# Kernel optimization log

Measured on AMD Instinct MI355X. Metric: run time of the kernel, lower is better.

## Reference

```python
import jax, jax.numpy as jnp
import numpy as np

N_DOC, N_WORD, N_ENT, N_POS = 10000, 20000, 10000, 60
D, D_POS_IN, D_WEMB = 128, 60, 300
E11, E22, E33, E01, E02, E03 = 320000, 160000, 3600, 300000, 100000, 150000
EPS = 1e-9


def spmm(rows, cols, vals, x, n_out):
    """Sparse (n_out x n_in) adjacency @ x via gather + weighted segment-sum."""
    return jax.ops.segment_sum(vals[:, None] * x[cols], rows, num_segments=n_out)


def gcn(rows, cols, vals, x, n_out, W=None, b=None):
    """GCN layer: adj @ (x W + b) with ReLU; identity=True in torch == W is None."""
    h = x if W is None else x @ W + b
    return jax.nn.relu(spmm(rows, cols, vals, h, n_out))


def setup_inputs():
    key = jax.random.key(0)
    ks = iter(jax.random.split(key, 64))
    randn = lambda s: jax.random.normal(next(ks), s, jnp.float32)
    rand = lambda s: jax.random.uniform(next(ks), s, dtype=jnp.float32)
    ridx = lambda s, hi: jax.random.randint(next(ks), s, 0, hi, jnp.int32)
    return {
        "f1": randn((N_WORD, D)),
        "f2": randn((N_ENT, D)),
        "f3": randn((N_POS, D_POS_IN)),
        "word_emb": randn((N_ENT, D_WEMB)),
        "a11_rows": ridx((E11,), N_WORD), "a11_cols": ridx((E11,), N_WORD), "a11_vals": rand((E11,)),
        "a22_rows": ridx((E22,), N_ENT), "a22_cols": ridx((E22,), N_ENT), "a22_vals": rand((E22,)),
        "a33_rows": ridx((E33,), N_POS), "a33_cols": ridx((E33,), N_POS), "a33_vals": rand((E33,)),
        "a01_rows": ridx((E01,), N_DOC), "a01_cols": ridx((E01,), N_WORD), "a01_vals": rand((E01,)),
        "a02_rows": ridx((E02,), N_DOC), "a02_cols": ridx((E02,), N_ENT), "a02_vals": rand((E02,)),
        "a03_rows": ridx((E03,), N_DOC), "a03_cols": ridx((E03,), N_POS), "a03_vals": rand((E03,)),
        "W3": randn((D_POS_IN, D)) * 0.1, "b3": jnp.zeros((D,), jnp.float32),
        "W1_2": randn((D, D)) * 0.1, "b1_2": jnp.zeros((D,), jnp.float32),
        "W2_2": randn((D, D)) * 0.1, "b2_2": jnp.zeros((D,), jnp.float32),
        "W3_2": randn((D, D)) * 0.1, "b3_2": jnp.zeros((D,), jnp.float32),
    }


def reference(f1, f2, f3, word_emb,
              a11_rows, a11_cols, a11_vals, a22_rows, a22_cols, a22_vals,
              a33_rows, a33_cols, a33_vals, a01_rows, a01_cols, a01_vals,
              a02_rows, a02_cols, a02_vals, a03_rows, a03_cols, a03_vals,
              W3, b3, W1_2, b1_2, W2_2, b2_2, W3_2, b3_2):
    # eval mode: F.dropout(training=False) is a no-op
    # type 1 (words): GCN(identity=True) -> GCN_2
    h1 = gcn(a11_rows, a11_cols, a11_vals, f1, N_WORD)
    h1 = gcn(a11_rows, a11_cols, a11_vals, h1, N_WORD, W1_2, b1_2)
    # type 2 (entities, concat_word_emb=True): GCN(identity=True) -> GCN_2 -> concat word_emb
    h2 = gcn(a22_rows, a22_cols, a22_vals, f2, N_ENT)
    h2 = gcn(a22_rows, a22_cols, a22_vals, h2, N_ENT, W2_2, b2_2)
    h2 = jnp.concatenate([h2, word_emb], axis=-1)  # [N_ENT, D + D_WEMB]
    # type 3 (POS): full GCN -> GCN_2
    h3 = gcn(a33_rows, a33_cols, a33_vals, f3, N_POS, W3, b3)
    h3 = gcn(a33_rows, a33_cols, a33_vals, h3, N_POS, W3_2, b3_2)
    # cross-type aggregation onto documents + L2 normalization
    outs = []
    for rows, cols, vals, h in ((a01_rows, a01_cols, a01_vals, h1),
                                (a02_rows, a02_cols, a02_vals, h2),
                                (a03_rows, a03_cols, a03_vals, h3)):
        agg = spmm(rows, cols, vals, h, N_DOC)  # [N_DOC, d]
        outs.append(agg / (jnp.linalg.norm(agg, axis=-1, keepdims=True) + EPS))
    return tuple(outs)
```

## Files before the change

### kernel.cpp

```cpp
#include <hip/hip_runtime.h>
#include <hip/hip_bf16.h>

typedef __hip_bfloat16 bf16;

#define N_DOC   10000
#define N_WORD  20000
#define N_ENT   10000
#define N_POS   60
#define DD      128
#define D_WEMB  300
#define E11     320000
#define E22     160000
#define E33     3600
#define E01     300000
#define E02     100000
#define E03     150000

#define ROFF11  0
#define ROFF22  20000
#define ROFF33  30000
#define ROFF01  30060
#define ROFF02  40060
#define ROFF03  50060
#define NROWS   60060
// ... 129 lines not shown
    int j = tid & 127;
    int row = row0 + q;
    float* xrh = xr + q * K;
    if (row < N_POS && j < K) {
        float x = loadf(X, (size_t)row * K + j, xisb);
        if (RELU) x = fmaxf(x, 0.f);
        xrh[j] = x;
    }
    __syncthreads();
    if (row >= N_POS) return;
    float acc = loadf(b, j, isb);
    #pragma unroll 8
    for (int k = 0; k < K; ++k)
        acc = fmaf(xrh[k], loadf(W, (size_t)k * 128 + j, isb), acc);
    storef(out, (size_t)row * 128 + j, oisb, acc);
}

__global__ __launch_bounds__(512) void bin_edges_fused(
        const int* __restrict__ r11, const int* __restrict__ c11, const void* __restrict__ v11,
        const int* __restrict__ r22, const int* __restrict__ c22, const void* __restrict__ v22,
        const int* __restrict__ r33, const int* __restrict__ c33, const void* __restrict__ v33,
        const int* __restrict__ r01, const int* __restrict__ c01, const void* __restrict__ v01,
        const int* __restrict__ r02, const int* __restrict__ c02, const void* __restrict__ v02,
        const int* __restrict__ r03, const int* __restrict__ c03, const void* __restrict__ v03,
        int* __restrict__ bcur, uint2* __restrict__ staging,
        const void* __restrict__ f1, const void* __restrict__ f2, const void* __restrict__ wemb,
        unsigned* __restrict__ f1q, unsigned* __restrict__ f2q, unsigned* __restrict__ wq,
        const void* __restrict__ f3, const void* __restrict__ W3, const void* __restrict__ b3,
        void* __restrict__ P3a,
        const int* __restrict__ dflag) {
    __shared__ int smem_i[3 * NBUCK];
    int* hist   = smem_i;
    int* gbase  = smem_i + NBUCK;
    int* cursor = smem_i + 2 * NBUCK;
    int blk = blockIdx.x;
    int t = threadIdx.x;
    if (blk < NB1K) {
        if (t < NBUCK) { hist[t] = 0; cursor[t] = 0; }
        __syncthreads();
        int isb = *dflag;
        int base0 = blk * P1_TILE;
        unsigned rx[P1_EPT], ry[P1_EPT];
        int bk[P1_EPT];
        #pragma unroll
        for (int k = 0; k < P1_EPT; ++k) {
            int i = base0 + t + k * 512;
            bk[k] = -1;
            if (i < NEDGES) {
                int slot, col; float val;
                edge_decode(i, r11, c11, v11, r22, c22, v22, r33, c33, v33,
                            r01, c01, v01, r02, c02, v02, r03, c03, v03,
                            isb, slot, col, val);
                rx[k] = ((unsigned)slot << 16) | (unsigned)col;
                ry[k] = f2b(val);
                bk[k] = slot >> BSHIFT;
                atomicAdd(&hist[bk[k]], 1);
            }
        }
        __syncthreads();
        if (t < NBUCK) {
            int c = hist[t];
            gbase[t] = c ? atomicAdd(bcur + t, c) : 0;
        }
        __syncthreads();
        #pragma unroll
        for (int k = 0; k < P1_EPT; ++k) {
            if (bk[k] >= 0) {
                int p = atomicAdd(&cursor[bk[k]], 1);
                int dst = gbase[bk[k]] + p;
                if (dst < (bk[k] + 1) * BCAP)
                    staging[dst] = make_uint2(rx[k], ry[k]);
            }
        }
    } else if (blk < NB1K + NCONV) {
        int isb = *dflag;
        int tid = (blk - NB1K) * 512 + t;
        int stride = NCONV * 512;
        conv_seg(f1,   f1q, N_WORD * (DD / 2),     isb, tid, stride);
        conv_seg(f2,   f2q, N_ENT  * (DD / 2),     isb, tid, stride);
        conv_seg(wemb, wq,  N_ENT  * (D_WEMB / 2), isb, tid, stride);
    } else {
        int isb = *dflag;
        int row0 = (blk - NB1K - NCONV) * 4;
        rowpar_body512<false, 60>(f3, isb, W3, b3, P3a, isb, isb, row0, t, (float*)smem_i);
    }
}

__global__ __launch_bounds__(512) void finalize_csr(
        const int* __restrict__ bcur, const uint2* __restrict__ staging,
        int* __restrict__ G, unsigned* __restrict__ pairs) {
    __shared__ int h[512], rp[512], cu[512];
    __shared__ int wsum2[8], wtop[2], bbs[2];
    int b = blockIdx.x, t = threadIdx.x;
    int lane = t & 63, w = t >> 6;
    h[t] = 0;
    int cnt_t = 0, s = 0;
    if (t < NBUCK) {
        int c = bcur[t] - t * BCAP;
        cnt_t = (c < BCAP) ? c : BCAP;
    }
    if (t < 128) {
        s = cnt_t;
        #pragma unroll
        for (int off = 1; off < 64; off <<= 1) {
            int y = __shfl_up(s, off);
            if (lane >= off) s += y;
        }
        if (lane == 63) wtop[w] = s;
    }
    __syncthreads();
    if (t == b) {
        bbs[0] = ((w > 0) ? wtop[0] : 0) + s - cnt_t;
        bbs[1] = cnt_t;
    }
    if (b == NBUCK - 1 && t == NBUCK - 1)
        G[NROWS] = ((w > 0) ? wtop[0] : 0) + s;
    __syncthreads();
    int bb = bbs[0];
    int cnt = bbs[1];
    const uint2* st = staging + (size_t)b * BCAP;
    for (int i = t; i < cnt; i += 512)
        atomicAdd(&h[(st[i].x >> 16) & 511], 1);
    __syncthreads();
    int x = h[t];
    s = x;
    #pragma unroll
    for (int off = 1; off < 64; off <<= 1) {
        int y = __shfl_up(s, off);
        if (lane >= off) s += y;
    }
    if (lane == 63) wsum2[w] = s;
    __syncthreads();
    if (t < 8) {
        int v = wsum2[t];
        #pragma unroll
        for (int off = 1; off < 8; off <<= 1) {
            int y = __shfl_up(v, off);
            if (lane >= off) v += y;
        }
        wsum2[t] = v;
    }
    __syncthreads();
    int myrp = ((w > 0) ? wsum2[w - 1] : 0) + s - x;
    rp[t] = myrp;
    cu[t] = 0;
    int slot = (b << BSHIFT) + t;
    if (slot < NROWS) G[slot] = bb + myrp;
    __syncthreads();
    for (int i = t; i < cnt; i += 512) {
        uint2 r = st[i];
        int sl = (r.x >> 16) & 511;
        int p = atomicAdd(&cu[sl], 1);
        pairs[bb + rp[sl] + p] = (r.y << 16) | (r.x & 0xffffu);
    }
}

__global__ void hist2_kernel(const int* __restrict__ rowsA, int nEA,
                             const int* __restrict__ rowsB, int nEB,
                             int nA, int* __restrict__ cnt) {
    int i = blockIdx.x * blockDim.x + threadIdx.x;
    if (i < nEA) atomicAdd(cnt + rowsA[i], 1);
    else if (i < nEA + nEB) atomicAdd(cnt + nA + rowsB[i - nEA], 1);
}

__device__ void scan_ex(const int* __restrict__ cnt, int* __restrict__ rp, int n) {
    __shared__ int wsum[16];
    __shared__ int carry;
    int t = threadIdx.x, lane = t & 63, w = t >> 6;
    if (t == 0) carry = 0;
    __syncthreads();
    for (int base = 0; base < n; base += 1024) {
        int i = base + t;
        int x = (i < n) ? cnt[i] : 0;
        int s = x;
        #pragma unroll
        for (int off = 1; off < 64; off <<= 1) {
            int y = __shfl_up(s, off);
            if (lane >= off) s += y;
        }
        if (lane == 63) wsum[w] = s;
        __syncthreads();
        if (w == 0) {
            int v = (lane < 16) ? wsum[lane] : 0;
            #pragma unroll
            for (int off = 1; off < 16; off <<= 1) {
                int y = __shfl_up(v, off);
                if (lane >= off) v += y;
            }
            if (lane < 16) wsum[lane] = v;
        }
        __syncthreads();
        int woff = (w > 0) ? wsum[w - 1] : 0;
        if (i < n) rp[i] = carry + woff + s - x;
        __syncthreads();
        if (t == 0) carry += wsum[15];
        __syncthreads();
    }
    if (t == 0) rp[n] = carry;
}

__global__ __launch_bounds__(1024) void scan2_kernel(
        const int* __restrict__ cntA, int* __restrict__ rpA, int nA,
        const int* __restrict__ cntB, int* __restrict__ rpB, int nB) {
    scan_ex(cntA, rpA, nA);
    __syncthreads();
    scan_ex(cntB, rpB, nB);
}

__global__ void copy2_kernel(const int* __restrict__ rpA, const int* __restrict__ rpB,
                             int nA, int nB, int* __restrict__ cur) {
    int i = blockIdx.x * blockDim.x + threadIdx.x;
    if (i < nA) cur[i] = rpA[i];
    else if (i < nA + nB) cur[i] = rpB[i - nA];
}

__global__ void scatter2_kernel(const int* __restrict__ rowsA, const int* __restrict__ colsA,
                                const void* __restrict__ valsA, int nEA,
                                const int* __restrict__ rowsB, const int* __restrict__ colsB,
                                const void* __restrict__ valsB, int nEB,
                                int nA, int* __restrict__ cur,
                                unsigned* __restrict__ pairsA, unsigned* __restrict__ pairsB,
                                const int* __restrict__ dflag) {
    int i = blockIdx.x * blockDim.x + threadIdx.x;
    int isb = *dflag;
    if (i < nEA) {
        int p = atomicAdd(cur + rowsA[i], 1);
        pairsA[p] = pack_pair(colsA[i], loadf(valsA, i, isb));
    } else if (i < nEA + nEB) {
        int k = i - nEA;
        int p = atomicAdd(cur + nA + rowsB[k], 1);
        pairsB[p] = pack_pair(colsB[k], loadf(valsB, k, isb));
    }
}

template<bool RELU>
__device__ __forceinline__ void gather_accum16(
        const int* __restrict__ rp, const unsigned* __restrict__ pairs,
        const void* __restrict__ src, int sisb, int row, int lane,
        float& tx, float& ty) {
    int e0 = rp[row], e1 = rp[row + 1];
    float accx[8], accy[8];
    #pragma unroll
    for (int k = 0; k < 8; ++k) { accx[k] = 0.f; accy[k] = 0.f; }
    int e = e0;
    if (sisb) {
        const bf16* sb = (const bf16*)src;
        for (; e + 16 <= e1; e += 16) {
            unsigned p[16], u[16];
            #pragma unroll
            for (int k = 0; k < 16; ++k) p[k] = pairs[e + k];
            #pragma unroll
            for (int k = 0; k < 16; ++k)
                u[k] = ((const unsigned*)(sb + (size_t)(p[k] & 0xffffu) * 128))[lane];
            #pragma unroll
            for (int k = 0; k < 16; ++k) {
                float v = b2f(p[k] >> 16);
                float x0 = b2f(u[k] & 0xffffu), x1 = b2f(u[k] >> 16);
                if (RELU) { x0 = fmaxf(x0, 0.f); x1 = fmaxf(x1, 0.f); }
                accx[k & 7] = fmaf(v, x0, accx[k & 7]);
                accy[k & 7] = fmaf(v, x1, accy[k & 7]);
            }
        }
        for (; e + 8 <= e1; e += 8) {
            unsigned p[8], u[8];
            #pragma unroll
            for (int k = 0; k < 8; ++k) p[k] = pairs[e + k];
            #pragma unroll
            for (int k = 0; k < 8; ++k)
                u[k] = ((const unsigned*)(sb + (size_t)(p[k] & 0xffffu) * 128))[lane];
            #pragma unroll
            for (int k = 0; k < 8; ++k) {
                float v = b2f(p[k] >> 16);
                float x0 = b2f(u[k] & 0xffffu), x1 = b2f(u[k] >> 16);
                if (RELU) { x0 = fmaxf(x0, 0.f); x1 = fmaxf(x1, 0.f); }
                accx[k] = fmaf(v, x0, accx[k]);
                accy[k] = fmaf(v, x1, accy[k]);
            }
        }
        for (; e + 2 <= e1; e += 2) {
            unsigned p0 = pairs[e], p1 = pairs[e + 1];
            unsigned u0 = ((const unsigned*)(sb + (size_t)(p0 & 0xffffu) * 128))[lane];
            unsigned u1 = ((const unsigned*)(sb + (size_t)(p1 & 0xffffu) * 128))[lane];
            float v0 = b2f(p0 >> 16), v1 = b2f(p1 >> 16);
            float x0 = b2f(u0 & 0xffffu), x1 = b2f(u0 >> 16);
            float y0 = b2f(u1 & 0xffffu), y1 = b2f(u1 >> 16);
            if (RELU) {
                x0 = fmaxf(x0, 0.f); x1 = fmaxf(x1, 0.f);
                y0 = fmaxf(y0, 0.f); y1 = fmaxf(y1, 0.f);
            }
            accx[0] = fmaf(v0, x0, accx[0]); accy[0] = fmaf(v0, x1, accy[0]);
            accx[1] = fmaf(v1, y0, accx[1]); accy[1] = fmaf(v1, y1, accy[1]);
        }
        if (e < e1) {
            unsigned p = pairs[e];
            float v = b2f(p >> 16);
            unsigned u = ((const unsigned*)(sb + (size_t)(p & 0xffffu) * 128))[lane];
            float x0 = b2f(u & 0xffffu), x1 = b2f(u >> 16);
            if (RELU) { x0 = fmaxf(x0, 0.f); x1 = fmaxf(x1, 0.f); }
            accx[0] = fmaf(v, x0, accx[0]); accy[0] = fmaf(v, x1, accy[0]);
        }
    } else {
        const float* sf = (const float*)src;
        for (; e + 16 <= e1; e += 16) {
            unsigned p[16]; float2 u[16];
            #pragma unroll
            for (int k = 0; k < 16; ++k) p[k] = pairs[e + k];
            #pragma unroll
            for (int k = 0; k < 16; ++k)
                u[k] = ((const float2*)(sf + (size_t)(p[k] & 0xffffu) * 128))[lane];
            #pragma unroll
            for (int k = 0; k < 16; ++k) {
                float v = b2f(p[k] >> 16);
                float x0 = u[k].x, x1 = u[k].y;
                if (RELU) { x0 = fmaxf(x0, 0.f); x1 = fmaxf(x1, 0.f); }
                accx[k & 7] = fmaf(v, x0, accx[k & 7]);
                accy[k & 7] = fmaf(v, x1, accy[k & 7]);
            }
        }
        for (; e + 8 <= e1; e += 8) {
            unsigned p[8]; float2 u[8];
            #pragma unroll
            for (int k = 0; k < 8; ++k) p[k] = pairs[e + k];
            #pragma unroll
            for (int k = 0; k < 8; ++k)
                u[k] = ((const float2*)(sf + (size_t)(p[k] & 0xffffu) * 128))[lane];
            #pragma unroll
            for (int k = 0; k < 8; ++k) {
                float v = b2f(p[k] >> 16);
                float x0 = u[k].x, x1 = u[k].y;
                if (RELU) { x0 = fmaxf(x0, 0.f); x1 = fmaxf(x1, 0.f); }
                accx[k] = fmaf(v, x0, accx[k]);
                accy[k] = fmaf(v, x1, accy[k]);
            }
        }
        for (; e + 2 <= e1; e += 2) {
            unsigned p0 = pairs[e], p1 = pairs[e + 1];
            float2 x = ((const float2*)(sf + (size_t)(p0 & 0xffffu) * 128))[lane];
            float2 y = ((const float2*)(sf + (size_t)(p1 & 0xffffu) * 128))[lane];
            float v0 = b2f(p0 >> 16), v1 = b2f(p1 >> 16);
            if (RELU) {
                x.x = fmaxf(x.x, 0.f); x.y = fmaxf(x.y, 0.f);
                y.x = fmaxf(y.x, 0.f); y.y = fmaxf(y.y, 0.f);
            }
            accx[0] = fmaf(v0, x.x, accx[0]); accy[0] = fmaf(v0, x.y, accy[0]);
            accx[1] = fmaf(v1, y.x, accx[1]); accy[1] = fmaf(v1, y.y, accy[1]);
        }
        if (e < e1) {
            unsigned p = pairs[e];
            float v = b2f(p >> 16);
            float2 x = ((const float2*)(sf + (size_t)(p & 0xffffu) * 128))[lane];
            if (RELU) { x.x = fmaxf(x.x, 0.f); x.y = fmaxf(x.y, 0.f); }
            accx[0] = fmaf(v, x.x, accx[0]); accy[0] = fmaf(v, x.y, accy[0]);
        }
    }
    tx = ((accx[0] + accx[1]) + (accx[2] + accx[3])) + ((accx[4] + accx[5]) + (accx[6] + accx[7]));
    ty = ((accy[0] + accy[1]) + (accy[2] + accy[3])) + ((accy[4] + accy[5]) + (accy[6] + accy[7]));
}

template<bool RELU>
__device__ __forceinline__ void gather128_body(
        const int* __restrict__ rp, const unsigned* __restrict__ pairs,
        const void* __restrict__ src, int sisb,
        void* __restrict__ dst, int disb, int row, int lane) {
    float tx, ty;
    gather_accum16<RELU>(rp, pairs, src, sisb, row, lane, tx, ty);
    if (disb) {
        ((unsigned*)((bf16*)dst + (size_t)row * 128))[lane] = f2b(tx) | (f2b(ty) << 16);
    } else {
        ((float2*)((float*)dst + (size_t)row * 128))[lane] = make_float2(tx, ty);
    }
}

template<bool RELU>
__device__ __forceinline__ void norm128_body(
        const int* __restrict__ rp, const unsigned* __restrict__ pairs,
        const void* __restrict__ src, int sisb,
        void* __restrict__ out, size_t elem_off, int row, int lane, int isb) {
    float tx, ty;
    gather_accum16<RELU>(rp, pairs, src, sisb, row, lane, tx, ty);
    float ss = tx * tx + ty * ty;
    #pragma unroll
    for (int off = 32; off > 0; off >>= 1) ss += __shfl_down(ss, off);
    ss = __shfl(ss, 0);
    float inv = 1.0f / (sqrtf(ss) + 1e-9f);
    size_t base = elem_off + (size_t)row * 128;
    if (isb) {
        ((unsigned*)((bf16*)out + base))[lane] = f2b(tx * inv) | (f2b(ty * inv) << 16);
    } else {
        ((float2*)((float*)out + base))[lane] = make_float2(tx * inv, ty * inv);
    }
}

__device__ __forceinline__ void norm428_body(
        const int* __restrict__ rp, const unsigned* __restrict__ pairs,
        const void* __restrict__ src1, int s1b,
        const void* __restrict__ src2, int s2b,
        void* __restrict__ out, size_t elem_off, int row, int lane, int isb) {
    constexpr int P2 = D_WEMB / 2;
    int e0 = rp[row], e1 = rp[row + 1];
    float2 a1 = make_float2(0.f, 0.f), b1 = make_float2(0.f, 0.f);
    float2 a2[3], b2v[3];
// ... 63 lines not shown
        }
        x0 = fmaxf(x0, 0.f); x1 = fmaxf(x1, 0.f);
        a1.x = fmaf(v, x0, a1.x); a1.y = fmaf(v, x1, a1.y);
        if (s2b) {
            const unsigned* sp = (const unsigned*)((const bf16*)src2 + (size_t)c * D_WEMB);
            #pragma unroll
            for (int s = 0; s < 3; ++s) {
                int pi = lane + 64 * s;
                if (pi < P2) {
                    unsigned u = sp[pi];
                    a2[s].x = fmaf(v, b2f(u & 0xffffu), a2[s].x);
                    a2[s].y = fmaf(v, b2f(u >> 16),     a2[s].y);
                }
            }
        } else {
            const float2* sp = (const float2*)((const float*)src2 + (size_t)c * D_WEMB);
            #pragma unroll
            for (int s = 0; s < 3; ++s) {
                int pi = lane + 64 * s;
                if (pi < P2) {
                    float2 x = sp[pi];
                    a2[s].x = fmaf(v, x.x, a2[s].x);
                    a2[s].y = fmaf(v, x.y, a2[s].y);
                }
            }
        }
    }
    float t1x = a1.x + b1.x, t1y = a1.y + b1.y;
    float t2x[3], t2y[3];
    #pragma unroll
    for (int s = 0; s < 3; ++s) { t2x[s] = a2[s].x + b2v[s].x; t2y[s] = a2[s].y + b2v[s].y; }
    float ss = t1x * t1x + t1y * t1y;
    #pragma unroll
    for (int s = 0; s < 3; ++s) {
        int pi = lane + 64 * s;
        if (pi < P2) ss += t2x[s] * t2x[s] + t2y[s] * t2y[s];
    }
    #pragma unroll
    for (int off = 32; off > 0; off >>= 1) ss += __shfl_down(ss, off);
    ss = __shfl(ss, 0);
    float inv = 1.0f / (sqrtf(ss) + 1e-9f);
    size_t base = elem_off + (size_t)row * (DD + D_WEMB);
    if (isb) {
        ((unsigned*)((bf16*)out + base))[lane] = f2b(t1x * inv) | (f2b(t1y * inv) << 16);
        unsigned* o2 = (unsigned*)((bf16*)out + base + DD);
        #pragma unroll
        for (int s = 0; s < 3; ++s) {
            int pi = lane + 64 * s;
            if (pi < P2) o2[pi] = f2b(t2x[s] * inv) | (f2b(t2y[s] * inv) << 16);
        }
    } else {
        ((float2*)((float*)out + base))[lane] = make_float2(t1x * inv, t1y * inv);
        float2* o2 = (float2*)((float*)out + base + DD);
        #pragma unroll
        for (int s = 0; s < 3; ++s) {
            int pi = lane + 64 * s;
            if (pi < P2) o2[pi] = make_float2(t2x[s] * inv, t2y[s] * inv);
        }
    }
}

template<bool RELU>
__global__ void spmm_gather128(const int* __restrict__ rowptr, const unsigned* __restrict__ pairs,
                               const void* __restrict__ src, int src_flagged,
                               void* __restrict__ dst, int dst_flagged,
                               int n, const int* __restrict__ dflag) {
    int row = blockIdx.x * 4 + (threadIdx.x >> 6);
    if (row >= n) return;
    int isb = *dflag;
    gather128_body<RELU>(rowptr, pairs, src, src_flagged ? isb : 0,
                         dst, dst_flagged ? isb : 0, row, threadIdx.x & 63);
}

__global__ void hop_posg(const int* __restrict__ G, const unsigned* __restrict__ pairs,
                         int roff1, const void* __restrict__ src1, void* __restrict__ dst1, int n1, int B1,
                         int roff2, const void* __restrict__ src2, void* __restrict__ dst2, int n2, int B2,
                         const void* __restrict__ Psrc, void* __restrict__ Pdst,
                         const int* __restrict__ dflag) {
    int b = blockIdx.x;
    int lane = threadIdx.x & 63;
    if (b < B1) {
        int row = b * 4 + (threadIdx.x >> 6);
        if (row >= n1) return;
        gather128_body<false>(G + roff1, pairs, src1, 1, dst1, 1, row, lane);
    } else if (b < B1 + B2) {
        int row = (b - B1) * 4 + (threadIdx.x >> 6);
        if (row >= n2) return;
        gather128_body<false>(G + roff2, pairs, src2, 1, dst2, 1, row, lane);
    } else {
        int isb = *dflag;
        int row = (b - B1 - B2) * 4 + (threadIdx.x >> 6);
        if (row >= N_POS) return;
        gather128_body<false>(G + ROFF33, pairs, Psrc, isb, Pdst, isb, row, lane);
    }
}

template<bool RELU>
__global__ void spmm_norm128(const int* __restrict__ rowptr, const unsigned* __restrict__ pairs,
                             const void* __restrict__ src, int src_flagged,
                             void* __restrict__ out, size_t elem_off,
                             int n, const int* __restrict__ dflag) {
    int row = blockIdx.x * 4 + (threadIdx.x >> 6);
    if (row >= n) return;
    int isb = *dflag;
    norm128_body<RELU>(rowptr, pairs, src, src_flagged ? isb : 0, out, elem_off,
                       row, threadIdx.x & 63, isb);
}

__global__ void spmm2_norm(const int* __restrict__ rowptr, const unsigned* __restrict__ pairs,
                           const void* __restrict__ src1, int s1_flagged,
                           const void* __restrict__ src2, int s2_flagged,
                           void* __restrict__ out, size_t elem_off,
                           int n, const int* __restrict__ dflag) {
    int row = blockIdx.x * 4 + (threadIdx.x >> 6);
    if (row >= n) return;
    int isb = *dflag;
    norm428_body(rowptr, pairs, src1, s1_flagged ? isb : 0, src2, s2_flagged ? isb : 0,
                 out, elem_off, row, threadIdx.x & 63, isb);
}

__global__ void final_norm_all(const int* __restrict__ G, const unsigned* __restrict__ pairs,
                               const void* __restrict__ s1, const void* __restrict__ e0b,
                               const void* __restrict__ wemb, const void* __restrict__ p3b,
                               void* __restrict__ out,
                               size_t off1, size_t off2, size_t off3,
                               const int* __restrict__ dflag) {
    int isb = *dflag;
    int lane = threadIdx.x & 63;
    int b = blockIdx.x;
    if (b < 2500) {
        int row = b * 4 + (threadIdx.x >> 6);
        if (row >= N_DOC) return;
        norm128_body<true>(G + ROFF01, pairs, s1, 1, out, off1, row, lane, isb);
    } else if (b < 5000) {
        int row = (b - 2500) * 4 + (threadIdx.x >> 6);
        if (row >= N_DOC) return;
        norm428_body(G + ROFF02, pairs, e0b, 1, wemb, 1, out, off2, row, lane, isb);
    } else {
        int row = (b - 5000) * 4 + (threadIdx.x >> 6);
        if (row >= N_DOC) return;
        norm128_body<true>(G + ROFF03, pairs, p3b, isb, out, off3, row, lane, isb);
    }
}

template<bool RELU>
__global__ void spmm_kernel(const int* __restrict__ rows, const int* __restrict__ cols,
                            const void* __restrict__ vals,
                            const void* __restrict__ src, int sstride, int src_flagged,
                            float* __restrict__ dst, int dstride, int doff,
                            int d, int nE, const int* __restrict__ dflag) {
    int e = blockIdx.x * (blockDim.x >> 6) + (threadIdx.x >> 6);
    if (e >= nE) return;
    int isb  = *dflag;
    int sisb = src_flagged ? isb : 0;
    int lane = threadIdx.x & 63;
    int r = rows[e];
    int c = cols[e];
    float v = loadf(vals, e, isb);
    size_t sbase = (size_t)c * sstride;
    float* dp = dst + (size_t)r * dstride + doff;
    if (sisb) {
        const unsigned* sp = (const unsigned*)((const bf16*)src + sbase);
        for (int j = 2 * lane; j < d; j += 128) {
            unsigned u = sp[j >> 1];
            float x0 = b2f(u & 0xffffu);
            float x1 = b2f(u >> 16);
            if (RELU) { x0 = fmaxf(x0, 0.f); x1 = fmaxf(x1, 0.f); }
            atomicAdd(dp + j,     v * x0);
            atomicAdd(dp + j + 1, v * x1);
        }
    } else {
        const float2* sp = (const float2*)((const float*)src + sbase);
        for (int j = 2 * lane; j < d; j += 128) {
            float2 x = sp[j >> 1];
            if (RELU) { x.x = fmaxf(x.x, 0.f); x.y = fmaxf(x.y, 0.f); }
            atomicAdd(dp + j,     v * x.x);
            atomicAdd(dp + j + 1, v * x.y);
        }
    }
}

template<bool RELU, bool XB>
__device__ __forceinline__ void gemm_tile_body(
        const void* __restrict__ X, const void* __restrict__ W,
        const void* __restrict__ b, void* __restrict__ out, int n,
        int bx, int by, int isb, int oisb, float* Wl ) {
    if (bx * 64 >= n) return;
    int tid = threadIdx.x;
    int jc = by * 64;
    if (isb) {
        const uint2* Wg = (const uint2*)W;
        float4* Wl4 = (float4*)Wl;
        for (int vidx = tid; vidx < 2048; vidx += 256) {
            int k = vidx >> 4, jl4 = vidx & 15;
            uint2 u = Wg[k * 32 + (jc >> 2) + jl4];
            float4 vv;
            vv.x = b2f(u.x & 0xffffu);
            vv.y = b2f(u.x >> 16);
            vv.z = b2f(u.y & 0xffffu);
            vv.w = b2f(u.y >> 16);
            Wl4[vidx] = vv;
        }
    } else {
        const float4* Wg = (const float4*)W;
        float4* Wl4 = (float4*)Wl;
        for (int vidx = tid; vidx < 2048; vidx += 256) {
            int k = vidx >> 4, jl4 = vidx & 15;
            Wl4[vidx] = Wg[k * 32 + (jc >> 2) + jl4];
        }
    }
    __syncthreads();
    int j2 = tid & 31;
    int g  = tid >> 5;
    float bc0 = loadf(b, jc + 2 * j2, isb);
    float bc1 = loadf(b, jc + 2 * j2 + 1, isb);
    int i0 = bx * 64 + g * 8;
    float a0[8], a1[8];
    #pragma unroll
    for (int r = 0; r < 8; ++r) { a0[r] = bc0; a1[r] = bc1; }
    const char* xbase = (const char*)X + (size_t)i0 * 128 * (XB ? 2 : 4);
    const float2* Wl2 = (const float2*)Wl;
    #pragma unroll 2
    for (int k4 = 0; k4 < 32; ++k4) {
        float2 w0 = Wl2[(4 * k4 + 0) * 32 + j2];
        float2 w1 = Wl2[(4 * k4 + 1) * 32 + j2];
        float2 w2 = Wl2[(4 * k4 + 2) * 32 + j2];
        float2 w3 = Wl2[(4 * k4 + 3) * 32 + j2];
        #pragma unroll
        for (int r = 0; r < 8; ++r) {
            float4 v;
            if (XB) {
                uint2 u = ((const uint2*)xbase)[r * 32 + k4];
                v.x = b2f(u.x & 0xffffu); v.y = b2f(u.x >> 16);
                v.z = b2f(u.y & 0xffffu); v.w = b2f(u.y >> 16);
            } else {
                v = ((const float4*)xbase)[r * 32 + k4];
            }
            if (RELU) {
                v.x = fmaxf(v.x, 0.f); v.y = fmaxf(v.y, 0.f);
                v.z = fmaxf(v.z, 0.f); v.w = fmaxf(v.w, 0.f);
            }
            a0[r] = fmaf(v.w, w3.x, fmaf(v.z, w2.x, fmaf(v.y, w1.x, fmaf(v.x, w0.x, a0[r]))));
            a1[r] = fmaf(v.w, w3.y, fmaf(v.z, w2.y, fmaf(v.y, w1.y, fmaf(v.x, w0.y, a1[r]))));
        }
    }
    #pragma unroll
    for (int r = 0; r < 8; ++r) {
        int i = i0 + r;
        if (i < n) {
            if (oisb) {
                ((unsigned*)((bf16*)out + (size_t)i * 128 + jc))[j2] =
                    f2b(a0[r]) | (f2b(a1[r]) << 16);
            } else {
                ((float2*)((float*)out + (size_t)i * 128 + jc))[j2] =
                    make_float2(a0[r], a1[r]);
            }
        }
    }
}

template<bool RELU>
__global__ __launch_bounds__(256) void gemm_tile(
        const float* __restrict__ X, const void* __restrict__ W,
        const void* __restrict__ b, void* __restrict__ out, int n,
        const int* __restrict__ dflag) {
    __shared__ float Wl[128 * 64];
    int isb = *dflag;
    gemm_tile_body<RELU, false>(X, W, b, out, n, blockIdx.x, blockIdx.y, isb, isb, Wl);
}

template<bool RELU>
__global__ __launch_bounds__(256) void gemm_tile_b2g(
        const void* __restrict__ X1, const void* __restrict__ W1, const void* __restrict__ b1,
        void* __restrict__ out1, int n1, int G1,
        const void* __restrict__ X2, const void* __restrict__ W2, const void* __restrict__ b2,
        void* __restrict__ out2, int n2, int GT,
        const void* __restrict__ PX, const void* __restrict__ PW,
        const void* __restrict__ Pb, void* __restrict__ PO,
        const int* __restrict__ dflag) {
    __shared__ float Wl[128 * 64];
    int isb = *dflag;
    int x = blockIdx.x;
    if (x < G1) {
        gemm_tile_body<RELU, true>(X1, W1, b1, out1, n1, x, blockIdx.y, isb, 1, Wl);
    } else if (x < GT) {
        gemm_tile_body<RELU, true>(X2, W2, b2, out2, n2, x - G1, blockIdx.y, isb, 1, Wl);
    } else {
        if (blockIdx.y != 0) return;
        int row = (x - GT) * 2 + (threadIdx.x >> 7);
        rowpar_body256<true, 128>(PX, isb, PW, Pb, PO, isb, isb, row, threadIdx.x, Wl);
    }
}

template<bool RELU>
__global__ __launch_bounds__(256) void gemm128_kernel(
        const float* __restrict__ X, const void* __restrict__ W,
        const void* __restrict__ b, float* __restrict__ out, int n,
        const int* __restrict__ dflag) {
    __shared__ float Wl[128 * 128];
    int isb = *dflag;
    int tid = threadIdx.x;
    if (isb) {
        const uint2* Wg = (const uint2*)W;
        float4* Wl4 = (float4*)Wl;
        for (int idx = tid; idx < 4096; idx += 256) {
            uint2 u = Wg[idx];
            float4 vv;
            vv.x = b2f(u.x & 0xffffu);
            vv.y = b2f(u.x >> 16);
            vv.z = b2f(u.y & 0xffffu);
            vv.w = b2f(u.y >> 16);
            Wl4[idx] = vv;
        }
    } else {
        const float4* Wg = (const float4*)W;
        float4* Wl4 = (float4*)Wl;
        for (int idx = tid; idx < 4096; idx += 256) Wl4[idx] = Wg[idx];
    }
    __syncthreads();
    int j = tid & 127;
    int h = tid >> 7;
    float bj = loadf(b, j, isb);
    int row0 = blockIdx.x * 64 + h * 32;
    for (int q = 0; q < 8; ++q) {
        int gi = row0 + q * 4;
        if (gi >= n) break;
        const float4* x0 = (const float4*)(X + (size_t)gi * 128);
        const float4* x1 = x0 + 32;
        const float4* x2 = x1 + 32;
        const float4* x3 = x2 + 32;
        float a0 = bj, a1 = bj, a2 = bj, a3 = bj;
        #pragma unroll 4
        for (int k4 = 0; k4 < 32; ++k4) {
            float4 v0 = x0[k4], v1 = x1[k4], v2 = x2[k4], v3 = x3[k4];
            if (RELU) {
                v0.x = fmaxf(v0.x, 0.f); v0.y = fmaxf(v0.y, 0.f); v0.z = fmaxf(v0.z, 0.f); v0.w = fmaxf(v0.w, 0.f);
                v1.x = fmaxf(v1.x, 0.f); v1.y = fmaxf(v1.y, 0.f); v1.z = fmaxf(v1.z, 0.f); v1.w = fmaxf(v1.w, 0.f);
                v2.x = fmaxf(v2.x, 0.f); v2.y = fmaxf(v2.y, 0.f); v2.z = fmaxf(v2.z, 0.f); v2.w = fmaxf(v2.w, 0.f);
                v3.x = fmaxf(v3.x, 0.f); v3.y = fmaxf(v3.y, 0.f); v3.z = fmaxf(v3.z, 0.f); v3.w = fmaxf(v3.w, 0.f);
            }
            float w0 = Wl[(4 * k4 + 0) * 128 + j];
            float w1 = Wl[(4 * k4 + 1) * 128 + j];
            float w2 = Wl[(4 * k4 + 2) * 128 + j];
            float w3 = Wl[(4 * k4 + 3) * 128 + j];
            a0 = fmaf(v0.w, w3, fmaf(v0.z, w2, fmaf(v0.y, w1, fmaf(v0.x, w0, a0))));
            a1 = fmaf(v1.w, w3, fmaf(v1.z, w2, fmaf(v1.y, w1, fmaf(v1.x, w0, a1))));
            a2 = fmaf(v2.w, w3, fmaf(v2.z, w2, fmaf(v2.y, w1, fmaf(v2.x, w0, a2))));
            a3 = fmaf(v3.w, w3, fmaf(v3.z, w2, fmaf(v3.y, w1, fmaf(v3.x, w0, a3))));
        }
        float* o = out + (size_t)gi * 128 + j;
        o[0] = a0; o[128] = a1; o[256] = a2; o[384] = a3;
    }
}

template<bool RELU, int K>
__global__ void rowpar_gemm(const void* __restrict__ X, int x_flagged,
                            const void* __restrict__ W, const void* __restrict__ b,
                            void* __restrict__ out, int out_flagged,
                            const int* __restrict__ dflag) {
    __shared__ float xr[K];
    int isb  = *dflag;
    int xisb = x_flagged ? isb : 0;
    int oisb = out_flagged ? isb : 0;
    int row = blockIdx.x;
    int j = threadIdx.x;
    if (j < K) {
        float x = loadf(X, (size_t)row * K + j, xisb);
        if (RELU) x = fmaxf(x, 0.f);
        xr[j] = x;
    }
    __syncthreads();
    float acc = loadf(b, j, isb);
    #pragma unroll 8
// ... 71 lines not shown
        for (int j = 2 * lane; j < d; j += 128) {
            float2 x = a2[j >> 1];
            o[j >> 1] = make_float2(x.x * inv, x.y * inv);
        }
    }
}

static inline int spmm_grid(int nE) { return (nE + 3) / 4; }
static inline int row_grid(int n)   { return (n + 3) / 4; }
static inline int pad8(int x)       { return (x + 7) & ~7; }

static void build2(hipStream_t stream,
                   const int* rowsA, const int* colsA, const void* valsA, int nA, int nEA,
                   const int* rowsB, const int* colsB, const void* valsB, int nB, int nEB,
                   int* rpA, int* rpB, int* curAB, unsigned* pairsA, unsigned* pairsB,
                   const int* dflag) {
    int nE = nEA + nEB;
    hipMemsetAsync(curAB, 0, (size_t)(nA + nB) * 4, stream);
    hist2_kernel<<<(nE + 255) / 256, 256, 0, stream>>>(rowsA, nEA, rowsB, nEB, nA, curAB);
    scan2_kernel<<<1, 1024, 0, stream>>>(curAB, rpA, nA, curAB + nA, rpB, nB);
    copy2_kernel<<<(nA + nB + 255) / 256, 256, 0, stream>>>(rpA, rpB, nA, nB, curAB);
    scatter2_kernel<<<(nE + 255) / 256, 256, 0, stream>>>(
        rowsA, colsA, valsA, nEA, rowsB, colsB, valsB, nEB, nA, curAB, pairsA, pairsB, dflag);
}

extern "C" void kernel_launch(void* const* d_in, const int* in_sizes, int n_in,
                              void* d_out, int out_size, void* d_ws, size_t ws_size,
                              hipStream_t stream) {
    const void* f1   = d_in[0];
    const void* f2   = d_in[1];
    const void* f3   = d_in[2];
    const void* wemb = d_in[3];
    const int*  a11r = (const int*)d_in[4];
    const int*  a11c = (const int*)d_in[5];
    const void* a11v = d_in[6];
    const int*  a22r = (const int*)d_in[7];
    const int*  a22c = (const int*)d_in[8];
    const void* a22v = d_in[9];
    const int*  a33r = (const int*)d_in[10];
    const int*  a33c = (const int*)d_in[11];
    const void* a33v = d_in[12];
    const int*  a01r = (const int*)d_in[13];
    const int*  a01c = (const int*)d_in[14];
    const void* a01v = d_in[15];
    const int*  a02r = (const int*)d_in[16];
    const int*  a02c = (const int*)d_in[17];
    const void* a02v = d_in[18];
    const int*  a03r = (const int*)d_in[19];
    const int*  a03c = (const int*)d_in[20];
    const void* a03v = d_in[21];
    const void* W3   = d_in[22];
    const void* b3   = d_in[23];
    const void* W1_2 = d_in[24];
    const void* b1_2 = d_in[25];
    const void* W2_2 = d_in[26];
    const void* b2_2 = d_in[27];
    const void* W3_2 = d_in[28];
    const void* b3_2 = d_in[29];

    int*   dflag = (int*)d_ws;
    float* base  = (float*)d_ws + 16;

    const size_t OUT1_OFF = 0;
    const size_t OUT2_OFF = (size_t)N_DOC * DD;
    const size_t OUT3_OFF = OUT2_OFF + (size_t)N_DOC * (DD + D_WEMB);

    dim3 blk(256);

    const size_t WS_BIG = 64 + (size_t)HFO_END * 4;
    const size_t WS_MID = 64 + 22240000ull + (60008ull + 620000ull) * 4;

    if (ws_size >= WS_BIG) {
        uint2*    staging = (uint2*)(base + HFO_STAGE);
        unsigned* pairs   = (unsigned*)(base + HFO_PAIRS);
        int*      G       = (int*)(base + HFO_G);
        int*      bcur    = (int*)(base + HFO_BCUR);
        void*     f1q     = (void*)(base + HFO_F1B);
        void*     f2q     = (void*)(base + HFO_F2B);
        void*     wq      = (void*)(base + HFO_WEMBB);
        void*     S0b     = (void*)(base + HFO_S0B);
        void*     S1b     = (void*)(base + HFO_S1B);
        void*     E0b     = (void*)(base + HFO_E0B);
        void*     E1b     = (void*)(base + HFO_E1B);
        float*    P3a     = base + HFO_P3A;
        float*    P3b     = base + HFO_P3B;

        detect_kernel<<<1, 256, 0, stream>>>((const unsigned*)f1, dflag, bcur);

        bin_edges_fused<<<NB1K + NCONV + NPOSB1, 512, 0, stream>>>(
            a11r, a11c, a11v, a22r, a22c, a22v, a33r, a33c, a33v,
            a01r, a01c, a01v, a02r, a02c, a02v, a03r, a03c, a03v,
            bcur, staging,
            f1, f2, wemb, (unsigned*)f1q, (unsigned*)f2q, (unsigned*)wq,
            f3, W3, b3, P3a, dflag);

        finalize_csr<<<NBUCK, 512, 0, stream>>>(bcur, staging, G, pairs);

        int B1 = row_grid(N_WORD), B2 = row_grid(N_ENT);
        hop_posg<<<B1 + B2 + row_grid(N_POS), blk, 0, stream>>>(
            G, pairs, ROFF11, f1q, S0b, N_WORD, B1,
            ROFF22, f2q, E0b, N_ENT, B2, P3a, P3b, dflag);
        {
            int G1 = pad8((N_WORD + 63) / 64), G2 = pad8((N_ENT + 63) / 64);
            int GT = G1 + G2;
            gemm_tile_b2g<true><<<dim3(GT + 30, 2), 256, 0, stream>>>(
                S0b, W1_2, b1_2, S1b, N_WORD, G1,
                E0b, W2_2, b2_2, E1b, N_ENT, GT,
                P3b, W3_2, b3_2, P3a, dflag);
        }
        hop_posg<<<B1 + B2 + row_grid(N_POS), blk, 0, stream>>>(
            G, pairs, ROFF11, S1b, S0b, N_WORD, B1,
            ROFF22, E1b, E0b, N_ENT, B2, P3a, P3b, dflag);

        final_norm_all<<<7500, blk, 0, stream>>>(
            G, pairs, S0b, E0b, wq, P3b, d_out, OUT1_OFF, OUT2_OFF, OUT3_OFF, dflag);
    } else if (ws_size >= WS_MID) {
        detect_kernel<<<1, 256, 0, stream>>>((const unsigned*)f1, dflag, (int*)nullptr);
        float* S0   = base;
        float* S1   = base + 2560000;
        float* E0   = base;
        float* E1   = base + 1280000;
        float* P3a  = base;
        float* P3b  = base + 7680;
        int* I = (int*)(base + 5560000);
        {
            int* rpA = I; int* rpB = rpA + (N_WORD + 1); int* cur = rpB + (N_DOC + 1);
            unsigned* pA = (unsigned*)(cur + N_WORD + N_DOC); unsigned* pB = pA + E11;
            build2(stream, a11r, a11c, a11v, N_WORD, E11,
                   a01r, a01c, a01v, N_DOC, E01, rpA, rpB, cur, pA, pB, dflag);
            spmm_gather128<false><<<row_grid(N_WORD), blk, 0, stream>>>(
                rpA, pA, f1, 1, S0, 0, N_WORD, dflag);
            gemm_tile<true><<<dim3(pad8((N_WORD + 63) / 64), 2), 256, 0, stream>>>(
                S0, W1_2, b1_2, S1, N_WORD, dflag);
            spmm_gather128<false><<<row_grid(N_WORD), blk, 0, stream>>>(
                rpA, pA, S1, 1, S0, 1, N_WORD, dflag);
            spmm_norm128<true><<<row_grid(N_DOC), blk, 0, stream>>>(
                rpB, pB, S0, 1, d_out, OUT1_OFF, N_DOC, dflag);
        }
        {
            int* rpA = I; int* rpB = rpA + (N_ENT + 1); int* cur = rpB + (N_DOC + 1);
            unsigned* pA = (unsigned*)(cur + N_ENT + N_DOC); unsigned* pB = pA + E22;
            build2(stream, a22r, a22c, a22v, N_ENT, E22,
                   a02r, a02c, a02v, N_DOC, E02, rpA, rpB, cur, pA, pB, dflag);
            spmm_gather128<false><<<row_grid(N_ENT), blk, 0, stream>>>(
                rpA, pA, f2, 1, E0, 0, N_ENT, dflag);
            gemm_tile<true><<<dim3(pad8((N_ENT + 63) / 64), 2), 256, 0, stream>>>(
                E0, W2_2, b2_2, E1, N_ENT, dflag);
            spmm_gather128<false><<<row_grid(N_ENT), blk, 0, stream>>>(
                rpA, pA, E1, 1, E0, 1, N_ENT, dflag);
            spmm2_norm<<<row_grid(N_DOC), blk, 0, stream>>>(
                rpB, pB, E0, 1, wemb, 1, d_out, OUT2_OFF, N_DOC, dflag);
        }
        {
            int* rpA = I; int* rpB = rpA + (N_POS + 1); int* cur = rpB + (N_DOC + 1);
            unsigned* pA = (unsigned*)(cur + N_POS + N_DOC); unsigned* pB = pA + E33;
            build2(stream, a33r, a33c, a33v, N_POS, E33,
                   a03r, a03c, a03v, N_DOC, E03, rpA, rpB, cur, pA, pB, dflag);
            rowpar_gemm<false, 60><<<N_POS, 128, 0, stream>>>(
                f3, 1, W3, b3, P3a, 1, dflag);
            spmm_gather128<false><<<row_grid(N_POS), blk, 0, stream>>>(
                rpA, pA, P3a, 1, P3b, 1, N_POS, dflag);
            rowpar_gemm<true, 128><<<N_POS, 128, 0, stream>>>(
                P3b, 1, W3_2, b3_2, P3a, 1, dflag);
            spmm_gather128<false><<<row_grid(N_POS), blk, 0, stream>>>(
                rpA, pA, P3a, 1, P3b, 1, N_POS, dflag);
            spmm_norm128<true><<<row_grid(N_DOC), blk, 0, stream>>>(
                rpB, pB, P3b, 1, d_out, OUT3_OFF, N_DOC, dflag);
        }
// ... 58 lines not shown
```

Measured before the change: 286.8 us.

## Use 16-byte quarter-wave gathers for bf16 SpMM rows and store POS features as bf16

Adds gather4 helpers in which each wavefront splits into four 16-lane groups. Each group loads a whole 256-byte bf16 row with uint4 loads, and the partial sums are combined with cross-lane shuffles. This replaces the old scheme where each lane loaded 4 bytes per edge, and it is used for the hop gathers and two of the normalization paths. The POS intermediates are now always written and read as bf16, whatever the input dtype, so the new path applies to them too. The 16-edge unrolled loops in the old gather are dropped. Wider loads mean fewer memory transactions, at the cost of shuffle reductions, tail masking and extra bf16 rounding on the POS path.

```diff
diff --git a/kernel.cpp b/kernel.cpp
--- a/kernel.cpp
+++ b/kernel.cpp
@@ -235,7 +235,7 @@
     } else {
         int isb = *dflag;
         int row0 = (blk - NB1K - NCONV) * 4;
-        rowpar_body512<false, 60>(f3, isb, W3, b3, P3a, isb, isb, row0, t, (float*)smem_i);
+        rowpar_body512<false, 60>(f3, isb, W3, b3, P3a, 1, isb, row0, t, (float*)smem_i);
     }
 }
 
@@ -386,6 +386,112 @@
     }
 }
 
+__device__ __forceinline__ void accum8_bf16(uint4 u, float v, bool relu, float* acc) {
+    float x0 = b2f(u.x & 0xffffu), x1 = b2f(u.x >> 16);
+    float x2 = b2f(u.y & 0xffffu), x3 = b2f(u.y >> 16);
+    float x4 = b2f(u.z & 0xffffu), x5 = b2f(u.z >> 16);
+    float x6 = b2f(u.w & 0xffffu), x7 = b2f(u.w >> 16);
+    if (relu) {
+        x0 = fmaxf(x0, 0.f); x1 = fmaxf(x1, 0.f); x2 = fmaxf(x2, 0.f); x3 = fmaxf(x3, 0.f);
+        x4 = fmaxf(x4, 0.f); x5 = fmaxf(x5, 0.f); x6 = fmaxf(x6, 0.f); x7 = fmaxf(x7, 0.f);
+    }
+    acc[0] = fmaf(v, x0, acc[0]); acc[1] = fmaf(v, x1, acc[1]);
+    acc[2] = fmaf(v, x2, acc[2]); acc[3] = fmaf(v, x3, acc[3]);
+    acc[4] = fmaf(v, x4, acc[4]); acc[5] = fmaf(v, x5, acc[5]);
+    acc[6] = fmaf(v, x6, acc[6]); acc[7] = fmaf(v, x7, acc[7]);
+}
+
+template<bool RELU>
+__device__ __forceinline__ void gather4_accum(
+        const int* __restrict__ rp, const unsigned* __restrict__ pairs,
+        const bf16* __restrict__ src, int row, int lane, float* acc) {
+    #pragma unroll
+    for (int j = 0; j < 8; ++j) acc[j] = 0.f;
+    int e0 = rp[row], e1 = rp[row + 1];
+    if (e0 >= e1) return;
+    int q = lane >> 4, sub = lane & 15;
+    int e = e0;
+    for (; e + 16 <= e1; e += 16) {
+        unsigned p0 = pairs[e + q];
+        unsigned p1 = pairs[e + 4 + q];
+        unsigned p2 = pairs[e + 8 + q];
+        unsigned p3 = pairs[e + 12 + q];
+        uint4 u0 = *(const uint4*)((const unsigned short*)src + (size_t)(p0 & 0xffffu) * 128 + sub * 8);
+        uint4 u1 = *(const uint4*)((const unsigned short*)src + (size_t)(p1 & 0xffffu) * 128 + sub * 8);
+        uint4 u2 = *(const uint4*)((const unsigned short*)src + (size_t)(p2 & 0xffffu) * 128 + sub * 8);
+        uint4 u3 = *(const uint4*)((const unsigned short*)src + (size_t)(p3 & 0xffffu) * 128 + sub * 8);
+        accum8_bf16(u0, b2f(p0 >> 16), RELU, acc);
+        accum8_bf16(u1, b2f(p1 >> 16), RELU, acc);
+        accum8_bf16(u2, b2f(p2 >> 16), RELU, acc);
+        accum8_bf16(u3, b2f(p3 >> 16), RELU, acc);
+    }
+    for (; e < e1; e += 4) {
+        int idx = e + q;
+        unsigned p = pairs[(idx < e1) ? idx : (e1 - 1)];
+        float v = (idx < e1) ? b2f(p >> 16) : 0.f;
+        uint4 u = *(const uint4*)((const unsigned short*)src + (size_t)(p & 0xffffu) * 128 + sub * 8);
+        accum8_bf16(u, v, RELU, acc);
+    }
+}
+
+template<bool RELU>
+__device__ __forceinline__ void gather4_body(
+        const int* __restrict__ rp, const unsigned* __restrict__ pairs,
+        const bf16* __restrict__ src, bf16* __restrict__ dst, int row, int lane) {
+    float acc[8];
+    gather4_accum<RELU>(rp, pairs, src, row, lane, acc);
+    #pragma unroll
+    for (int j = 0; j < 8; ++j) {
+        acc[j] += __shfl_xor(acc[j], 16);
+        acc[j] += __shfl_xor(acc[j], 32);
+    }
+    if ((lane >> 4) == 0) {
+        int sub = lane & 15;
+        uint4 o;
+        o.x = f2b(acc[0]) | (f2b(acc[1]) << 16);
+        o.y = f2b(acc[2]) | (f2b(acc[3]) << 16);
+        o.z = f2b(acc[4]) | (f2b(acc[5]) << 16);
+        o.w = f2b(acc[6]) | (f2b(acc[7]) << 16);
+        *(uint4*)((unsigned short*)dst + (size_t)row * 128 + sub * 8) = o;
+    }
+}
+
+template<bool RELU>
+__device__ __forceinline__ void norm4_body(
+        const int* __restrict__ rp, const unsigned* __restrict__ pairs,
+        const bf16* __restrict__ src, void* __restrict__ out, size_t elem_off,
+        int row, int lane, int oisb) {
+    float acc[8];
+    gather4_accum<RELU>(rp, pairs, src, row, lane, acc);
+    #pragma unroll
+    for (int j = 0; j < 8; ++j) {
+        acc[j] += __shfl_xor(acc[j], 16);
+        acc[j] += __shfl_xor(acc[j], 32);
+    }
+    float ss = 0.f;
+    #pragma unroll
+    for (int j = 0; j < 8; ++j) ss = fmaf(acc[j], acc[j], ss);
+    #pragma unroll
+    for (int off = 1; off < 16; off <<= 1) ss += __shfl_xor(ss, off);
+    float inv = 1.0f / (sqrtf(ss) + 1e-9f);
+    if ((lane >> 4) == 0) {
+        int sub = lane & 15;
+        size_t base = elem_off + (size_t)row * 128;
+        if (oisb) {
+            uint4 o;
+            o.x = f2b(acc[0] * inv) | (f2b(acc[1] * inv) << 16);
+            o.y = f2b(acc[2] * inv) | (f2b(acc[3] * inv) << 16);
+            o.z = f2b(acc[4] * inv) | (f2b(acc[5] * inv) << 16);
+            o.w = f2b(acc[6] * inv) | (f2b(acc[7] * inv) << 16);
+            *(uint4*)((unsigned short*)out + base + sub * 8) = o;
+        } else {
+            float4* op = (float4*)((float*)out + base);
+            op[sub * 2]     = make_float4(acc[0] * inv, acc[1] * inv, acc[2] * inv, acc[3] * inv);
+            op[sub * 2 + 1] = make_float4(acc[4] * inv, acc[5] * inv, acc[6] * inv, acc[7] * inv);
+        }
+    }
+}
+
 template<bool RELU>
 __device__ __forceinline__ void gather_accum16(
         const int* __restrict__ rp, const unsigned* __restrict__ pairs,
@@ -398,22 +504,6 @@
     int e = e0;
     if (sisb) {
         const bf16* sb = (const bf16*)src;
-        for (; e + 16 <= e1; e += 16) {
-            unsigned p[16], u[16];
-            #pragma unroll
-            for (int k = 0; k < 16; ++k) p[k] = pairs[e + k];
-            #pragma unroll
-            for (int k = 0; k < 16; ++k)
-                u[k] = ((const unsigned*)(sb + (size_t)(p[k] & 0xffffu) * 128))[lane];
-            #pragma unroll
-            for (int k = 0; k < 16; ++k) {
-                float v = b2f(p[k] >> 16);
-                float x0 = b2f(u[k] & 0xffffu), x1 = b2f(u[k] >> 16);
-                if (RELU) { x0 = fmaxf(x0, 0.f); x1 = fmaxf(x1, 0.f); }
-                accx[k & 7] = fmaf(v, x0, accx[k & 7]);
-                accy[k & 7] = fmaf(v, x1, accy[k & 7]);
-            }
-        }
         for (; e + 8 <= e1; e += 8) {
             unsigned p[8], u[8];
             #pragma unroll
@@ -454,22 +544,6 @@
         }
     } else {
         const float* sf = (const float*)src;
-        for (; e + 16 <= e1; e += 16) {
-            unsigned p[16]; float2 u[16];
-            #pragma unroll
-            for (int k = 0; k < 16; ++k) p[k] = pairs[e + k];
-            #pragma unroll
-            for (int k = 0; k < 16; ++k)
-                u[k] = ((const float2*)(sf + (size_t)(p[k] & 0xffffu) * 128))[lane];
-            #pragma unroll
-            for (int k = 0; k < 16; ++k) {
-                float v = b2f(p[k] >> 16);
-                float x0 = u[k].x, x1 = u[k].y;
-                if (RELU) { x0 = fmaxf(x0, 0.f); x1 = fmaxf(x1, 0.f); }
-                accx[k & 7] = fmaf(v, x0, accx[k & 7]);
-                accy[k & 7] = fmaf(v, x1, accy[k & 7]);
-            }
-        }
         for (; e + 8 <= e1; e += 8) {
             unsigned p[8]; float2 u[8];
             #pragma unroll
@@ -699,16 +773,15 @@
     if (b < B1) {
         int row = b * 4 + (threadIdx.x >> 6);
         if (row >= n1) return;
-        gather128_body<false>(G + roff1, pairs, src1, 1, dst1, 1, row, lane);
+        gather4_body<false>(G + roff1, pairs, (const bf16*)src1, (bf16*)dst1, row, lane);
     } else if (b < B1 + B2) {
         int row = (b - B1) * 4 + (threadIdx.x >> 6);
         if (row >= n2) return;
-        gather128_body<false>(G + roff2, pairs, src2, 1, dst2, 1, row, lane);
+        gather4_body<false>(G + roff2, pairs, (const bf16*)src2, (bf16*)dst2, row, lane);
     } else {
-        int isb = *dflag;
         int row = (b - B1 - B2) * 4 + (threadIdx.x >> 6);
         if (row >= N_POS) return;
-        gather128_body<false>(G + ROFF33, pairs, Psrc, isb, Pdst, isb, row, lane);
+        gather4_body<false>(G + ROFF33, pairs, (const bf16*)Psrc, (bf16*)Pdst, row, lane);
     }
 }
 
@@ -748,7 +821,7 @@
     if (b < 2500) {
         int row = b * 4 + (threadIdx.x >> 6);
         if (row >= N_DOC) return;
-        norm128_body<true>(G + ROFF01, pairs, s1, 1, out, off1, row, lane, isb);
+        norm4_body<true>(G + ROFF01, pairs, (const bf16*)s1, out, off1, row, lane, isb);
     } else if (b < 5000) {
         int row = (b - 2500) * 4 + (threadIdx.x >> 6);
         if (row >= N_DOC) return;
@@ -756,7 +829,7 @@
     } else {
         int row = (b - 5000) * 4 + (threadIdx.x >> 6);
         if (row >= N_DOC) return;
-        norm128_body<true>(G + ROFF03, pairs, p3b, isb, out, off3, row, lane, isb);
+        norm4_body<true>(G + ROFF03, pairs, (const bf16*)p3b, out, off3, row, lane, isb);
     }
 }
 
@@ -905,7 +978,7 @@
     } else {
         if (blockIdx.y != 0) return;
         int row = (x - GT) * 2 + (threadIdx.x >> 7);
-        rowpar_body256<true, 128>(PX, isb, PW, Pb, PO, isb, isb, row, threadIdx.x, Wl);
+        rowpar_body256<true, 128>(PX, 1, PW, Pb, PO, 1, isb, row, threadIdx.x, Wl);
     }
 }
 
@@ -1143,8 +1216,8 @@
         void*     S1b     = (void*)(base + HFO_S1B);
         void*     E0b     = (void*)(base + HFO_E0B);
         void*     E1b     = (void*)(base + HFO_E1B);
-        float*    P3a     = base + HFO_P3A;
-        float*    P3b     = base + HFO_P3B;
+        void*     P3a     = (void*)(base + HFO_P3A);
+        void*     P3b     = (void*)(base + HFO_P3B);
 
         detect_kernel<<<1, 256, 0, stream>>>((const unsigned*)f1, dflag, bcur);
 
```

New measurement: 276.2 us. -3.7%, faster.
